# Optimization experiments

Hardware: AMD Instinct MI355X
Metric: run time of the kernel (lower is better)

The kernel has to match this reference:

```python
import jax, jax.numpy as jnp
import numpy as np
from jax import lax

DN = ('NCHW', 'OIHW', 'NCHW')


def squash(x):
    # x: [..., d]; squared-norm over last dim
    sq = jnp.sum(x * x, axis=-1, keepdims=True)
    return sq * x / ((1.0 + sq) * jnp.sqrt(sq))


def setup_inputs() -> dict:
    key = jax.random.key(0)
    ks = jax.random.split(key, 6)
    B = 512
    x = jax.random.normal(ks[0], (B, 1, 28, 28), dtype=jnp.float32)
    conv1_w = jax.random.normal(ks[1], (256, 1, 9, 9), dtype=jnp.float32) * 0.05
    conv1_b = jnp.zeros((256,), dtype=jnp.float32)
    conv2_w = jax.random.normal(ks[2], (256, 256, 9, 9), dtype=jnp.float32) * 0.02
    conv2_b = jnp.zeros((256,), dtype=jnp.float32)
    # W: [num_routes=1152, num_capsules=10, out_channels=16, in_channels=8]
    W = jax.random.normal(ks[3], (1152, 10, 16, 8), dtype=jnp.float32)
    return {"x": x, "conv1_w": conv1_w, "conv1_b": conv1_b,
            "conv2_w": conv2_w, "conv2_b": conv2_b, "W": W}


def reference(x, conv1_w, conv1_b, conv2_w, conv2_b, W):
    B = x.shape[0]
    # conv1 + ReLU: [B,1,28,28] -> [B,256,20,20]
    h = lax.conv_general_dilated(x, conv1_w, (1, 1), 'VALID', dimension_numbers=DN)
    h = jax.nn.relu(h + conv1_b[None, :, None, None])
    # primary capsule conv: [B,256,20,20] -> [B,256,6,6], stride 2
    h = lax.conv_general_dilated(h, conv2_w, (2, 2), 'VALID', dimension_numbers=DN)
    h = h + conv2_b[None, :, None, None]
    # reshape to capsules [B, 1152, 8] (matches torch .view on NCHW) and squash
    u = squash(h.reshape(B, -1, 8))
    # u_hat[b,r,c,o] = W[r,c,o,i] @ u[b,r,i]
    u_hat = jnp.einsum('rcoi,bri->brco', W, u)  # [B,1152,10,16]
    R, C = W.shape[0], W.shape[1]
    b_ij = jnp.zeros((R, C), dtype=x.dtype)
    num_iterations = 3
    for it in range(num_iterations):
        c_ij = jax.nn.softmax(b_ij, axis=0)          # softmax over routes
        s_j = jnp.einsum('rc,brco->bco', c_ij, u_hat)  # [B,10,16]
        v_j = squash(s_j)
        if it < num_iterations - 1:
            a_ij = jnp.einsum('brco,bco->brc', u_hat, v_j)  # agreement
            b_ij = b_ij + a_ij.mean(axis=0)
    return v_j  # [B,10,16]
```

## Files before the change

kernel.cpp:

```cpp
#include <hip/hip_runtime.h>
#include <stdint.h>


typedef unsigned short u16;
typedef unsigned int u32;
typedef _Float16 half8 __attribute__((ext_vector_type(8)));
typedef float f32x4 __attribute__((ext_vector_type(4)));

__device__ __forceinline__ u16 f2h(float f) {
  union { _Float16 h; u16 u; } cv;
  cv.h = (_Float16)f;
  return cv.u;
}

__device__ __forceinline__ void gload_lds16(const void* g, void* l) {
  __builtin_amdgcn_global_load_lds(
      (const __attribute__((address_space(1))) void*)g,
      (__attribute__((address_space(3))) void*)l, 16, 0, 0);
}

__global__ __launch_bounds__(256, 2) void conv1_kernel(
    const float* __restrict__ x, const float* __restrict__ w1,
    const float* __restrict__ b1, u16* __restrict__ hT) {
  int t = threadIdx.x;
  if (t >= 200) return;
  int bloc = t / 100, pos = t - bloc * 100;
  int b = blockIdx.x * 2 + bloc;
  int co0 = blockIdx.y * 128;
  int oh2 = pos / 10, ow2 = pos - oh2 * 10;
  const float* xb = x + (size_t)b * 784 + (2 * oh2) * 28 + 2 * ow2;
  float patch[10][10];
#pragma unroll
  for (int ky = 0; ky < 10; ++ky)
#pragma unroll
    for (int kx = 0; kx < 10; ++kx) patch[ky][kx] = xb[ky * 28 + kx];
  u16* hb = hT + ((size_t)b * 400 + (2 * oh2) * 20 + 2 * ow2) * 256 + co0;
  for (int c8 = 0; c8 < 16; ++c8) {
    u32 q00[4], q01[4], q10[4], q11[4];
#pragma unroll
    for (int cc = 0; cc < 8; ++cc) {
      int co = co0 + c8 * 8 + cc;
      const float* wc = w1 + co * 81;
      float a00 = 0.f, a01 = 0.f, a10 = 0.f, a11 = 0.f;
#pragma unroll
      for (int ky = 0; ky < 9; ++ky)
#pragma unroll
        for (int kx = 0; kx < 9; ++kx) {
          float wv = wc[ky * 9 + kx];
          a00 = fmaf(wv, patch[ky][kx], a00);
          a01 = fmaf(wv, patch[ky][kx + 1], a01);
          a10 = fmaf(wv, patch[ky + 1][kx], a10);
          a11 = fmaf(wv, patch[ky + 1][kx + 1], a11);
        }
      float bias = b1[co];
      u32 v00 = f2h(fmaxf(a00 + bias, 0.f));
      u32 v01 = f2h(fmaxf(a01 + bias, 0.f));
      u32 v10 = f2h(fmaxf(a10 + bias, 0.f));
      u32 v11 = f2h(fmaxf(a11 + bias, 0.f));
      if (cc & 1) {
        q00[cc >> 1] |= v00 << 16; q01[cc >> 1] |= v01 << 16;
        q10[cc >> 1] |= v10 << 16; q11[cc >> 1] |= v11 << 16;
      } else {
        q00[cc >> 1] = v00; q01[cc >> 1] = v01;
        q10[cc >> 1] = v10; q11[cc >> 1] = v11;
      }
    }
    *(uint4*)(hb + c8 * 8)        = make_uint4(q00[0], q00[1], q00[2], q00[3]);
    *(uint4*)(hb + 256 + c8 * 8)  = make_uint4(q01[0], q01[1], q01[2], q01[3]);
    *(uint4*)(hb + 5120 + c8 * 8) = make_uint4(q10[0], q10[1], q10[2], q10[3]);
    *(uint4*)(hb + 5376 + c8 * 8) = make_uint4(q11[0], q11[1], q11[2], q11[3]);
  }
}

__global__ __launch_bounds__(256) void prep_w2_kernel(
    const float* __restrict__ w2, u16* __restrict__ A2) {
  __shared__ u16 tl[81 * 264];
  int co = blockIdx.x;
  int tid = threadIdx.x;
  const float* wp = w2 + (size_t)co * 20736;
#pragma unroll
  for (int k = 0; k < 81; ++k) {
    int li = k * 256 + tid;
    int ci = li / 81, t = li - ci * 81;
    tl[t * 264 + ci] = f2h(wp[li]);
  }
  __syncthreads();
  u16* op = A2 + (size_t)co * 20736;
  for (int oc = tid; oc < 2592; oc += 256) {
    int k0 = oc * 8;
    int t = k0 >> 8, ci0 = k0 & 255;
    *(uint4*)(op + k0) = *(const uint4*)&tl[t * 264 + ci0];
  }
}

__global__ __launch_bounds__(256) void init_u_kernel(
    const float* __restrict__ b2, float* __restrict__ u) {
  int i = blockIdx.x * 256 + threadIdx.x;
  int b = i / 2304, j0 = (i - b * 2304) * 4;
  float4 v;
  v.x = b2[j0 / 36]; v.y = b2[(j0 + 1) / 36];
  v.z = b2[(j0 + 2) / 36]; v.w = b2[(j0 + 3) / 36];
  *(float4*)(u + (size_t)b * 9216 + j0) = v;
}

__global__ __launch_bounds__(512, 2) void conv2_kernel(
    const u16* __restrict__ hT, const u16* __restrict__ A2,
    float* __restrict__ u) {
  __shared__ __align__(16) u16 lds_[65536];
  char* const ldsc = (char*)lds_;
  const int bx = blockIdx.x;
  const int nbk = bx % 72, kz = bx / 72;
  const int n0 = nbk * 256;
  const int tid = threadIdx.x;
  const int lane = tid & 63, w = tid >> 6;
  const int wr = w >> 2, wc = w & 3;
  const int fr = lane & 15, fg = lane >> 4;
  const int w1024 = w * 1024;

  const int rA = tid >> 3;
  const int qsrc = (tid & 7) ^ (rA & 7);
  const int AbaseT = rA * 20736 + qsrc * 8;
  int Bb[4];
#pragma unroll
  for (int rg = 0; rg < 4; ++rg) {
    int n = n0 + rg * 64 + rA;
    int b = n / 36, sp = n - b * 36, oh = sp / 6, ow = sp - oh * 6;
    Bb[rg] = (b * 400 + oh * 40 + ow * 2) * 256 + qsrc * 8;
  }

  const int kx0 = (fg ^ (fr & 7)) << 4;
  const int kx1 = ((4 + fg) ^ (fr & 7)) << 4;
  const int wr16384 = wr * 16384;
  const int bh16384 = 32768 + (wc >> 1) * 16384;
  const int brow0 = (wc & 1) * 64;

  f32x4 acc[8][4] = {};
  half8 areg[4][2], breg[2][2];

#define STAGE_A(E, H, GT) do {                                               \
    char* p_ = ldsc + (E) * 65536 + (H) * 16384 + w1024;                     \
    gload_lds16(A2 + AbaseT + ((H) * 2 + 0) * 1327104 + (GT) * 64, p_);      \
    gload_lds16(A2 + AbaseT + ((H) * 2 + 1) * 1327104 + (GT) * 64, p_ + 8192); \
  } while (0)
#define STAGE_B(E, H, BOFF) do {                                             \
    char* p_ = ldsc + (E) * 65536 + 32768 + (H) * 16384 + w1024;             \
    gload_lds16(hT + Bb[(H) * 2 + 0] + (BOFF), p_);                          \
    gload_lds16(hT + Bb[(H) * 2 + 1] + (BOFF), p_ + 8192);                   \
  } while (0)
#define STAGE_ALL(E, GT) do {                                                \
    int tap_ = (GT) >> 2;                                                    \
    int kh_ = tap_ / 9, kw_ = tap_ - kh_ * 9;                                \
    int bo_ = (kh_ * 20 + kw_) * 256 + ((GT) & 3) * 64;                      \
    STAGE_A(E, 0, GT); STAGE_B(E, 0, bo_);                                   \
    STAGE_B(E, 1, bo_); STAGE_A(E, 1, GT);                                   \
  } while (0)
#define RD_A(D, MH) do { _Pragma("unroll")                                   \
    for (int mr = 0; mr < 4; ++mr) {                                         \
      const char* r_ = ldsc + (D) * 65536 + wr16384 +                        \
                       ((MH) * 64 + mr * 16 + fr) * 128;                     \
      areg[mr][0] = *(const half8*)(r_ + kx0);                               \
      areg[mr][1] = *(const half8*)(r_ + kx1);                               \
    } } while (0)
#define RD_B(D, NH) do { _Pragma("unroll")                                   \
    for (int nr = 0; nr < 2; ++nr) {                                         \
      const char* r_ = ldsc + (D) * 65536 + bh16384 +                        \
                       (brow0 + (NH) * 32 + nr * 16 + fr) * 128;             \
      breg[nr][0] = *(const half8*)(r_ + kx0);                               \
      breg[nr][1] = *(const half8*)(r_ + kx1);                               \
    } } while (0)
#define MM16(MH, NH) do {                                                    \
    __builtin_amdgcn_s_setprio(1);                                           \
    _Pragma("unroll") for (int mr = 0; mr < 4; ++mr)                         \
    _Pragma("unroll") for (int nr = 0; nr < 2; ++nr) {                       \
      acc[(MH)*4+mr][(NH)*2+nr] = __builtin_amdgcn_mfma_f32_16x16x32_f16(    \
          areg[mr][0], breg[nr][0], acc[(MH)*4+mr][(NH)*2+nr], 0, 0, 0);     \
      acc[(MH)*4+mr][(NH)*2+nr] = __builtin_amdgcn_mfma_f32_16x16x32_f16(    \
          areg[mr][1], breg[nr][1], acc[(MH)*4+mr][(NH)*2+nr], 0, 0, 0);     \
    }                                                                        \
    __builtin_amdgcn_s_setprio(0);                                           \
  } while (0)
#define BAR_PRE() do {                                                       \
    __builtin_amdgcn_s_barrier();                                            \
    asm volatile("s_waitcnt lgkmcnt(0)" ::: "memory");                       \
    __builtin_amdgcn_sched_barrier(0);                                       \
  } while (0)
#define BAR_ONLY() do {                                                      \
    __builtin_amdgcn_s_barrier();                                            \
    asm volatile("" ::: "memory");                                           \
  } while (0)
#define VM_BAR(N) do {                                                       \
    asm volatile("s_waitcnt vmcnt(" N ")" ::: "memory");                     \
    __builtin_amdgcn_s_barrier();                                            \
    asm volatile("" ::: "memory");                                           \
  } while (0)
#define TILE_STD(T, D, E) do {                                               \
    RD_A(D, 0); RD_B(D, 0);                                                  \
    STAGE_ALL(E, kz * 108 + (T) + 1);                                        \
    BAR_PRE(); MM16(0, 0); BAR_ONLY();                                       \
    RD_B(D, 1);                                                              \
    BAR_PRE(); MM16(0, 1); VM_BAR("8");                                      \
    RD_A(D, 1);                                                              \
    BAR_PRE(); MM16(1, 1); BAR_ONLY();                                       \
    RD_B(D, 0);                                                              \
    BAR_PRE(); MM16(1, 0); VM_BAR("2");                                      \
  } while (0)
#define TILE_LAST(D) do {                                                    \
    RD_A(D, 0); RD_B(D, 0);                                                  \
    BAR_PRE(); MM16(0, 0); BAR_ONLY();                                       \
    RD_B(D, 1);                                                              \
    BAR_PRE(); MM16(0, 1); VM_BAR("0");                                      \
    RD_A(D, 1);                                                              \
    BAR_PRE(); MM16(1, 1); BAR_ONLY();                                       \
    RD_B(D, 0);                                                              \
    BAR_PRE(); MM16(1, 0);                                                   \
  } while (0)

  STAGE_ALL(0, kz * 108);
  asm volatile("s_waitcnt vmcnt(2)" ::: "memory");
  __builtin_amdgcn_s_barrier();
  asm volatile("" ::: "memory");

  for (int tt = 0; tt < 53; ++tt) {
    TILE_STD(2 * tt, 0, 1);
    TILE_STD(2 * tt + 1, 1, 0);
  }
  TILE_STD(106, 0, 1);
  TILE_LAST(1);

#pragma unroll
  for (int nf = 0; nf < 4; ++nf) {
    int cn = n0 + wc * 64 + nf * 16 + fr;
    int ob = cn / 36;
    int os = cn - ob * 36;
    float* op = u + (size_t)ob * 9216 + os;
#pragma unroll
    for (int mf = 0; mf < 8; ++mf) {
      int row0 = wr * 128 + mf * 16 + fg * 4;
#pragma unroll
      for (int qq = 0; qq < 4; ++qq)
        atomicAdd(op + (row0 + qq) * 36, acc[mf][nf][qq]);
    }
  }
#undef STAGE_A
#undef STAGE_B
#undef STAGE_ALL
#undef RD_A
#undef RD_B
#undef MM16
#undef BAR_PRE
#undef BAR_ONLY
#undef VM_BAR
#undef TILE_STD
#undef TILE_LAST
}

__global__ __launch_bounds__(256) void squash_kernel(
    const float* __restrict__ u, u16* __restrict__ ub) {
  int idx = blockIdx.x * 256 + threadIdx.x;
  const float* up = u + (size_t)idx * 8;
  float4 a = *(const float4*)up;
  float4 c = *(const float4*)(up + 4);
  float sq = a.x * a.x + a.y * a.y + a.z * a.z + a.w * a.w +
             c.x * c.x + c.y * c.y + c.z * c.z + c.w * c.w;
  float f = sqrtf(sq) / (1.0f + sq);
  u16 o[8];
  o[0] = f2h(a.x * f); o[1] = f2h(a.y * f);
  o[2] = f2h(a.z * f); o[3] = f2h(a.w * f);
  o[4] = f2h(c.x * f); o[5] = f2h(c.y * f);
  o[6] = f2h(c.z * f); o[7] = f2h(c.w * f);
  *(uint4*)(ub + (size_t)idx * 8) = *(uint4*)o;
}

__global__ __launch_bounds__(256) void transp_kernel(
    const u16* __restrict__ ub, u16* __restrict__ ubT) {
  __shared__ u16 tl[64][72];
  int ri0 = blockIdx.x * 64, b0 = blockIdx.y * 64;
  int tid = threadIdx.x;
  int br = tid >> 2, cq = tid & 3;
  const u16* ip = ub + (size_t)(b0 + br) * 9216 + ri0 + cq * 16;
  uint4 v0 = *(const uint4*)ip;
  uint4 v1 = *(const uint4*)(ip + 8);
  *(uint4*)&tl[br][cq * 16] = v0;
  *(uint4*)&tl[br][cq * 16 + 8] = v1;
  __syncthreads();
  int rr = tid >> 2, cb = tid & 3;
  u16 o0[8], o1[8];
#pragma unroll
  for (int j = 0; j < 8; ++j) {
    o0[j] = tl[cb * 16 + j][rr];
    o1[j] = tl[cb * 16 + 8 + j][rr];
  }
  u16* opp = ubT + (size_t)(ri0 + rr) * 512 + b0 + cb * 16;
  *(uint4*)opp = *(uint4*)o0;
  *(uint4*)(opp + 8) = *(uint4*)o1;
}

__global__ __launch_bounds__(256) void softmax_c_kernel(
    const float* __restrict__ bij, float* __restrict__ cT) {
  int c = blockIdx.x;
  int tid = threadIdx.x;
  __shared__ float red[256];
  float mx = -1e30f;
  for (int r = tid; r < 1152; r += 256) mx = fmaxf(mx, bij[r * 10 + c]);
  red[tid] = mx;
  __syncthreads();
  for (int s = 128; s > 0; s >>= 1) {
    if (tid < s) red[tid] = fmaxf(red[tid], red[tid + s]);
    __syncthreads();
  }
  mx = red[0];
  __syncthreads();
  float sum = 0.f;
  for (int r = tid; r < 1152; r += 256) sum += expf(bij[r * 10 + c] - mx);
  red[tid] = sum;
  __syncthreads();
  for (int s = 128; s > 0; s >>= 1) {
    if (tid < s) red[tid] += red[tid + s];
    __syncthreads();
  }
  float inv = 1.0f / red[0];
  for (int r = tid; r < 1152; r += 256)
    cT[c * 1152 + r] = expf(bij[r * 10 + c] - mx) * inv;
}

__global__ __launch_bounds__(256) void gemm_s_kernel(
    const float* __restrict__ W, const float* __restrict__ cT,
    const u16* __restrict__ ub, float* __restrict__ s) {
  __shared__ __align__(16) u16 Asl[160 * 72];
  __shared__ __align__(16) u16 Bsl[64 * 72];
  int nb = blockIdx.x & 7, kzi = blockIdx.x >> 3;
  int n0 = nb * 64, k0 = kzi * 256;
  int tid = threadIdx.x;
  int lane = tid & 63, wave = tid >> 6;
  int fr = lane & 15, fg = lane >> 4;

  f32x4 acc[10] = {};
#pragma unroll
  for (int st = 0; st < 4; ++st) {
    int kb = k0 + st * 64;
    __syncthreads();
#pragma unroll
    for (int j = 0; j < 5; ++j) {
      int c5 = tid + j * 256;
      int row = c5 >> 3, qq = c5 & 7;
      int cls = row >> 4, o = row & 15;
      int r = (kb + qq * 8) >> 3;
      const float* wp = W + (size_t)r * 1280 + cls * 128 + o * 8;
      float4 w0 = *(const float4*)wp;
      float4 w1 = *(const float4*)(wp + 4);
      float cs = cT[cls * 1152 + r] * 512.0f;
      u16 ov[8];
      ov[0] = f2h(w0.x * cs); ov[1] = f2h(w0.y * cs);
      ov[2] = f2h(w0.z * cs); ov[3] = f2h(w0.w * cs);
      ov[4] = f2h(w1.x * cs); ov[5] = f2h(w1.y * cs);
      ov[6] = f2h(w1.z * cs); ov[7] = f2h(w1.w * cs);
      *(uint4*)((char*)Asl + row * 144 + qq * 16) = *(uint4*)ov;
    }
#pragma unroll
    for (int j = 0; j < 2; ++j) {
      int c2 = tid + j * 256;
      int row = c2 >> 3, qq = c2 & 7;
      *(uint4*)((char*)Bsl + row * 144 + qq * 16) =
          *(const uint4*)(ub + (size_t)(n0 + row) * 9216 + kb + qq * 8);
    }
    __syncthreads();
#pragma unroll
    for (int s2 = 0; s2 < 2; ++s2) {
      int xg = (s2 * 4 + fg) * 16;
      half8 bf0 = *(const half8*)((char*)Bsl + (wave * 16 + fr) * 144 + xg);
#pragma unroll
      for (int m = 0; m < 10; ++m) {
        half8 af = *(const half8*)((char*)Asl + (m * 16 + fr) * 144 + xg);
        acc[m] = __builtin_amdgcn_mfma_f32_16x16x32_f16(af, bf0, acc[m], 0, 0, 0);
      }
    }
  }
  int bcol = n0 + wave * 16 + fr;
#pragma unroll
  for (int m = 0; m < 10; ++m)
#pragma unroll
    for (int qq = 0; qq < 4; ++qq)
      atomicAdd(s + (m * 16 + fg * 4 + qq) * 512 + bcol, acc[m][qq]);
}

__global__ __launch_bounds__(256) void squash_v_kernel(
    float* __restrict__ s, u16* __restrict__ vb,
    float* __restrict__ outp, int write_out) {
  int idx = blockIdx.x * 256 + threadIdx.x;
  int c = idx >> 9, b = idx & 511;
  float vals[16];
  float sq = 0.f;
#pragma unroll
  for (int o = 0; o < 16; ++o) {
    float v = s[(c * 16 + o) * 512 + b] * (1.0f / 512.0f);
    vals[o] = v;
    sq += v * v;
  }
#pragma unroll
  for (int o = 0; o < 16; ++o) s[(c * 16 + o) * 512 + b] = 0.f;
  float f = sqrtf(sq) / (1.0f + sq);
  if (write_out) {
#pragma unroll
    for (int o = 0; o < 16; ++o) outp[((size_t)b * 10 + c) * 16 + o] = vals[o] * f;
  } else {
#pragma unroll
    for (int o = 0; o < 16; ++o)
      vb[(c * 16 + o) * 512 + b] = f2h(vals[o] * f * 4096.0f);
  }
}

__global__ __launch_bounds__(256) void gemm_gc_kernel(
    const u16* __restrict__ vb, const u16* __restrict__ ubT,
    const float* __restrict__ W, float* __restrict__ bij) {
  __shared__ __align__(16) u16 Agl[160 * 72];
  __shared__ __align__(16) u16 Bgl[128 * 72];
  __shared__ float Gl[160 * 129];
  int nb = blockIdx.x % 72, kzi = blockIdx.x / 72;
  int n0 = nb * 128, k0 = kzi * 128;
  int tid = threadIdx.x;
  int lane = tid & 63, wave = tid >> 6;
  int fr = lane & 15, fg = lane >> 4;
  f32x4 acc[10][2] = {};
#pragma unroll
  for (int st = 0; st < 2; ++st) {
    int kb = k0 + st * 64;
    __syncthreads();
#pragma unroll
    for (int j = 0; j < 5; ++j) {
      int c5 = tid + j * 256;
      int row = c5 >> 3, qq = c5 & 7;
      *(uint4*)((char*)Agl + row * 144 + qq * 16) =
          *(const uint4*)(vb + (size_t)row * 512 + kb + qq * 8);
    }
#pragma unroll
    for (int j = 0; j < 4; ++j) {
      int c4 = tid + j * 256;
      int row = c4 >> 3, qq = c4 & 7;
      *(uint4*)((char*)Bgl + row * 144 + qq * 16) =
          *(const uint4*)(ubT + (size_t)(n0 + row) * 512 + kb + qq * 8);
    }
    __syncthreads();
#pragma unroll
    for (int s2 = 0; s2 < 2; ++s2) {
      int xg = (s2 * 4 + fg) * 16;
      half8 bfv[2];
#pragma unroll
      for (int nn = 0; nn < 2; ++nn)
        bfv[nn] = *(const half8*)((char*)Bgl + (wave * 32 + nn * 16 + fr) * 144 + xg);
#pragma unroll
      for (int m = 0; m < 10; ++m) {
        half8 af = *(const half8*)((char*)Agl + (m * 16 + fr) * 144 + xg);
#pragma unroll
        for (int nn = 0; nn < 2; ++nn)
          acc[m][nn] = __builtin_amdgcn_mfma_f32_16x16x32_f16(af, bfv[nn],
                                                             acc[m][nn], 0, 0, 0);
      }
    }
  }
#pragma unroll
  for (int m = 0; m < 10; ++m)
#pragma unroll
    for (int nn = 0; nn < 2; ++nn) {
      int col = wave * 32 + nn * 16 + fr;
#pragma unroll
      for (int qq = 0; qq < 4; ++qq)
        Gl[(m * 16 + fg * 4 + qq) * 129 + col] = acc[m][nn][qq];
    }
  __syncthreads();
  if (tid < 160) {
    int rl = tid / 10, c = tid - rl * 10;
    int r = (n0 >> 3) + rl;
    const float* wp = W + (size_t)r * 1280 + c * 128;
    float a = 0.f;
#pragma unroll 4
    for (int o = 0; o < 16; ++o) {
      const float* gp = &Gl[(c * 16 + o) * 129 + rl * 8];
#pragma unroll
      for (int i = 0; i < 8; ++i) a = fmaf(wp[o * 8 + i], gp[i], a);
    }
    atomicAdd(&bij[r * 10 + c], a * (1.0f / (512.0f * 4096.0f)));
  }
}

extern "C" void kernel_launch(void* const* d_in, const int* in_sizes, int n_in,
                              void* d_out, int out_size, void* d_ws, size_t ws_size,
                              hipStream_t stream) {
  const float* x  = (const float*)d_in[0];
  const float* w1 = (const float*)d_in[1];
  const float* b1 = (const float*)d_in[2];
  const float* w2 = (const float*)d_in[3];
  const float* b2 = (const float*)d_in[4];
  const float* W  = (const float*)d_in[5];
  char* ws = (char*)d_ws;
  u16*   hT  = (u16*)ws;
  u16*   A2  = (u16*)(ws + 104857600);
  float* u   = (float*)(ws + 115474432);
  float* bij = (float*)(ws + 134348800);
  float* cT  = (float*)(ws + 134394880);
  float* s   = (float*)(ws + 134440960);
  u16*   ub  = (u16*)ws;
  u16*   ubT = (u16*)(ws + 9437184);
  u16*   vb  = (u16*)(ws + 21823488);
  float* out = (float*)d_out;

  hipMemsetAsync(bij, 0, 46080, stream);
  hipMemsetAsync(s, 0, 327680, stream);
  init_u_kernel<<<4608, 256, 0, stream>>>(b2, u);
  conv1_kernel<<<dim3(256, 2), 256, 0, stream>>>(x, w1, b1, hT);
  prep_w2_kernel<<<256, 256, 0, stream>>>(w2, A2);
  conv2_kernel<<<216, 512, 0, stream>>>(hT, A2, u);
  squash_kernel<<<2304, 256, 0, stream>>>(u, ub);
  transp_kernel<<<dim3(144, 8), 256, 0, stream>>>(ub, ubT);
  for (int it = 0; it < 3; ++it) {
    softmax_c_kernel<<<10, 256, 0, stream>>>(bij, cT);
    gemm_s_kernel<<<288, 256, 0, stream>>>(W, cT, ub, s);
    squash_v_kernel<<<20, 256, 0, stream>>>(s, vb, out, it == 2 ? 1 : 0);
    if (it < 2) gemm_gc_kernel<<<288, 256, 0, stream>>>(vb, ubT, W, bij);
  }
}
```

Measured before the change: 642.0 us.

## Simplify conv1 to per-channel threads and compute final routing in fp32

```diff
diff --git a/kernel.cpp b/kernel.cpp
--- a/kernel.cpp
+++ b/kernel.cpp
@@ -19,56 +19,28 @@
       (__attribute__((address_space(3))) void*)l, 16, 0, 0);
 }
 
-__global__ __launch_bounds__(256, 2) void conv1_kernel(
+__global__ __launch_bounds__(256) void conv1_kernel(
     const float* __restrict__ x, const float* __restrict__ w1,
     const float* __restrict__ b1, u16* __restrict__ hT) {
-  int t = threadIdx.x;
-  if (t >= 200) return;
-  int bloc = t / 100, pos = t - bloc * 100;
-  int b = blockIdx.x * 2 + bloc;
-  int co0 = blockIdx.y * 128;
-  int oh2 = pos / 10, ow2 = pos - oh2 * 10;
-  const float* xb = x + (size_t)b * 784 + (2 * oh2) * 28 + 2 * ow2;
-  float patch[10][10];
-#pragma unroll
-  for (int ky = 0; ky < 10; ++ky)
-#pragma unroll
-    for (int kx = 0; kx < 10; ++kx) patch[ky][kx] = xb[ky * 28 + kx];
-  u16* hb = hT + ((size_t)b * 400 + (2 * oh2) * 20 + 2 * ow2) * 256 + co0;
-  for (int c8 = 0; c8 < 16; ++c8) {
-    u32 q00[4], q01[4], q10[4], q11[4];
-#pragma unroll
-    for (int cc = 0; cc < 8; ++cc) {
-      int co = co0 + c8 * 8 + cc;
-      const float* wc = w1 + co * 81;
-      float a00 = 0.f, a01 = 0.f, a10 = 0.f, a11 = 0.f;
+  int b = blockIdx.x;
+  int co = threadIdx.x;
+  float w[81];
+  const float* wp = w1 + co * 81;
+#pragma unroll
+  for (int k = 0; k < 81; ++k) w[k] = wp[k];
+  float bias = b1[co];
+  const float* xb = x + (size_t)b * 784;
+  u16* hb = hT + (size_t)b * 102400 + co;
+  for (int y = 0; y < 20; ++y) {
+    for (int xo = 0; xo < 20; ++xo) {
+      float acc = bias;
 #pragma unroll
       for (int ky = 0; ky < 9; ++ky)
 #pragma unroll
-        for (int kx = 0; kx < 9; ++kx) {
-          float wv = wc[ky * 9 + kx];
-          a00 = fmaf(wv, patch[ky][kx], a00);
-          a01 = fmaf(wv, patch[ky][kx + 1], a01);
-          a10 = fmaf(wv, patch[ky + 1][kx], a10);
-          a11 = fmaf(wv, patch[ky + 1][kx + 1], a11);
-        }
-      float bias = b1[co];
-      u32 v00 = f2h(fmaxf(a00 + bias, 0.f));
-      u32 v01 = f2h(fmaxf(a01 + bias, 0.f));
-      u32 v10 = f2h(fmaxf(a10 + bias, 0.f));
-      u32 v11 = f2h(fmaxf(a11 + bias, 0.f));
-      if (cc & 1) {
-        q00[cc >> 1] |= v00 << 16; q01[cc >> 1] |= v01 << 16;
-        q10[cc >> 1] |= v10 << 16; q11[cc >> 1] |= v11 << 16;
-      } else {
-        q00[cc >> 1] = v00; q01[cc >> 1] = v01;
-        q10[cc >> 1] = v10; q11[cc >> 1] = v11;
-      }
-    }
-    *(uint4*)(hb + c8 * 8)        = make_uint4(q00[0], q00[1], q00[2], q00[3]);
-    *(uint4*)(hb + 256 + c8 * 8)  = make_uint4(q01[0], q01[1], q01[2], q01[3]);
-    *(uint4*)(hb + 5120 + c8 * 8) = make_uint4(q10[0], q10[1], q10[2], q10[3]);
-    *(uint4*)(hb + 5376 + c8 * 8) = make_uint4(q11[0], q11[1], q11[2], q11[3]);
+        for (int kx = 0; kx < 9; ++kx)
+          acc = fmaf(w[ky * 9 + kx], xb[(y + ky) * 28 + xo + kx], acc);
+      hb[(y * 20 + xo) * 256] = f2h(fmaxf(acc, 0.f));
+    }
   }
 }
 
@@ -255,19 +227,21 @@
 }
 
 __global__ __launch_bounds__(256) void squash_kernel(
-    const float* __restrict__ u, u16* __restrict__ ub) {
+    float* __restrict__ u, u16* __restrict__ ub) {
   int idx = blockIdx.x * 256 + threadIdx.x;
-  const float* up = u + (size_t)idx * 8;
+  float* up = u + (size_t)idx * 8;
   float4 a = *(const float4*)up;
   float4 c = *(const float4*)(up + 4);
   float sq = a.x * a.x + a.y * a.y + a.z * a.z + a.w * a.w +
              c.x * c.x + c.y * c.y + c.z * c.z + c.w * c.w;
   float f = sqrtf(sq) / (1.0f + sq);
+  a.x *= f; a.y *= f; a.z *= f; a.w *= f;
+  c.x *= f; c.y *= f; c.z *= f; c.w *= f;
+  *(float4*)up = a;
+  *(float4*)(up + 4) = c;
   u16 o[8];
-  o[0] = f2h(a.x * f); o[1] = f2h(a.y * f);
-  o[2] = f2h(a.z * f); o[3] = f2h(a.w * f);
-  o[4] = f2h(c.x * f); o[5] = f2h(c.y * f);
-  o[6] = f2h(c.z * f); o[7] = f2h(c.w * f);
+  o[0] = f2h(a.x); o[1] = f2h(a.y); o[2] = f2h(a.z); o[3] = f2h(a.w);
+  o[4] = f2h(c.x); o[5] = f2h(c.y); o[6] = f2h(c.z); o[7] = f2h(c.w);
   *(uint4*)(ub + (size_t)idx * 8) = *(uint4*)o;
 }
 
@@ -384,8 +358,7 @@
 }
 
 __global__ __launch_bounds__(256) void squash_v_kernel(
-    float* __restrict__ s, u16* __restrict__ vb,
-    float* __restrict__ outp, int write_out) {
+    float* __restrict__ s, u16* __restrict__ vb) {
   int idx = blockIdx.x * 256 + threadIdx.x;
   int c = idx >> 9, b = idx & 511;
   float vals[16];
@@ -399,14 +372,9 @@
 #pragma unroll
   for (int o = 0; o < 16; ++o) s[(c * 16 + o) * 512 + b] = 0.f;
   float f = sqrtf(sq) / (1.0f + sq);
-  if (write_out) {
-#pragma unroll
-    for (int o = 0; o < 16; ++o) outp[((size_t)b * 10 + c) * 16 + o] = vals[o] * f;
-  } else {
-#pragma unroll
-    for (int o = 0; o < 16; ++o)
-      vb[(c * 16 + o) * 512 + b] = f2h(vals[o] * f * 4096.0f);
-  }
+#pragma unroll
+  for (int o = 0; o < 16; ++o)
+    vb[(c * 16 + o) * 512 + b] = f2h(vals[o] * f * 4096.0f);
 }
 
 __global__ __launch_bounds__(256) void gemm_gc_kernel(
@@ -480,6 +448,47 @@
     }
     atomicAdd(&bij[r * 10 + c], a * (1.0f / (512.0f * 4096.0f)));
   }
+}
+
+__global__ __launch_bounds__(256) void route_final_kernel(
+    const float* __restrict__ cT, const float* __restrict__ u,
+    const float* __restrict__ W, float* __restrict__ outp) {
+  int c = blockIdx.y, b0 = blockIdx.x * 16;
+  int tid = threadIdx.x, lb = tid >> 4, o = tid & 15;
+  __shared__ float us[16][32][8];
+  __shared__ float cs[32];
+  float acc = 0.f;
+  for (int r0 = 0; r0 < 1152; r0 += 32) {
+    __syncthreads();
+#pragma unroll
+    for (int j = 0; j < 4; ++j) {
+      int i4 = tid + j * 256;
+      int bb = i4 >> 6, rem = i4 & 63;
+      int rr = rem >> 1, hf = rem & 1;
+      *(float4*)&us[bb][rr][hf * 4] =
+          *(const float4*)&u[(size_t)(b0 + bb) * 9216 + (r0 + rr) * 8 + hf * 4];
+    }
+    if (tid < 32) cs[tid] = cT[c * 1152 + r0 + tid];
+    __syncthreads();
+#pragma unroll 4
+    for (int rr = 0; rr < 32; ++rr) {
+      const float* wp = W + ((size_t)(r0 + rr) * 10 + c) * 128 + o * 8;
+      float4 w0 = *(const float4*)wp;
+      float4 w1v = *(const float4*)(wp + 4);
+      float4 ua = *(const float4*)&us[lb][rr][0];
+      float4 ub4 = *(const float4*)&us[lb][rr][4];
+      float d = w0.x * ua.x + w0.y * ua.y + w0.z * ua.z + w0.w * ua.w +
+                w1v.x * ub4.x + w1v.y * ub4.y + w1v.z * ub4.z + w1v.w * ub4.w;
+      acc = fmaf(cs[rr], d, acc);
+    }
+  }
+  float sq = acc * acc;
+  sq += __shfl_xor(sq, 1, 64);
+  sq += __shfl_xor(sq, 2, 64);
+  sq += __shfl_xor(sq, 4, 64);
+  sq += __shfl_xor(sq, 8, 64);
+  float f = sqrtf(sq) / (1.0f + sq);
+  outp[((size_t)(b0 + lb) * 10 + c) * 16 + o] = acc * f;
 }
 
 extern "C" void kernel_launch(void* const* d_in, const int* in_sizes, int n_in,
@@ -506,15 +515,19 @@
   hipMemsetAsync(bij, 0, 46080, stream);
   hipMemsetAsync(s, 0, 327680, stream);
   init_u_kernel<<<4608, 256, 0, stream>>>(b2, u);
-  conv1_kernel<<<dim3(256, 2), 256, 0, stream>>>(x, w1, b1, hT);
+  conv1_kernel<<<512, 256, 0, stream>>>(x, w1, b1, hT);
   prep_w2_kernel<<<256, 256, 0, stream>>>(w2, A2);
   conv2_kernel<<<216, 512, 0, stream>>>(hT, A2, u);
   squash_kernel<<<2304, 256, 0, stream>>>(u, ub);
   transp_kernel<<<dim3(144, 8), 256, 0, stream>>>(ub, ubT);
   for (int it = 0; it < 3; ++it) {
     softmax_c_kernel<<<10, 256, 0, stream>>>(bij, cT);
-    gemm_s_kernel<<<288, 256, 0, stream>>>(W, cT, ub, s);
-    squash_v_kernel<<<20, 256, 0, stream>>>(s, vb, out, it == 2 ? 1 : 0);
-    if (it < 2) gemm_gc_kernel<<<288, 256, 0, stream>>>(vb, ubT, W, bij);
-  }
-}
+    if (it < 2) {
+      gemm_s_kernel<<<288, 256, 0, stream>>>(W, cT, ub, s);
+      squash_v_kernel<<<20, 256, 0, stream>>>(s, vb);
+      gemm_gc_kernel<<<288, 256, 0, stream>>>(vb, ubT, W, bij);
+    } else {
+      route_final_kernel<<<dim3(32, 10), 256, 0, stream>>>(cT, u, W, out);
+    }
+  }
+}
```

Measured after the change: 721.5 us. 1.12x slower.
